# Optimization experiments

Measured on AMD Instinct MI355X. Metric: run time of the kernel, lower is better.

Reference implementation:

```python
import jax, jax.numpy as jnp
import numpy as np

B, C, H, W = 2, 192, 96, 96
HEADS, DG, KH, KW = 12, 12, 3, 3
K = KH * KW
PAD, DIL = KH // 2, 1
MLP_HIDDEN = 2 * C  # mlp_ratio = 2


def setup_inputs() -> dict:
    key = jax.random.key(0)
    ks = jax.random.split(key, 14)
    s = 0.02
    return {
        "q": jax.random.normal(ks[0], (B, C, H, W), jnp.float32),
        "k": jax.random.normal(ks[1], (B, C, H, W), jnp.float32),
        "v": jax.random.normal(ks[2], (B, C, H, W), jnp.float32),
        "offset": jax.random.normal(ks[3], (B, DG * 2 * K, H, W), jnp.float32),
        "Wq": jax.random.normal(ks[4], (C, C), jnp.float32) * s,
        "bq": jax.random.normal(ks[5], (C,), jnp.float32) * s,
        "Wk": jax.random.normal(ks[6], (C, C), jnp.float32) * s,
        "bk": jax.random.normal(ks[7], (C,), jnp.float32) * s,
        "Wv": jax.random.normal(ks[8], (C, C), jnp.float32) * s,
        "bv": jax.random.normal(ks[9], (C,), jnp.float32) * s,
        "W1": jax.random.normal(ks[10], (C, MLP_HIDDEN), jnp.float32) * s,
        "b1": jax.random.normal(ks[11], (MLP_HIDDEN,), jnp.float32) * s,
        "W2": jax.random.normal(ks[12], (MLP_HIDDEN, C), jnp.float32) * s,
        "b2": jax.random.normal(ks[13], (C,), jnp.float32) * s,
    }


def _bilinear_sample(img, py, px):
    """img: [B,G,Cg,H,W]; py,px: [B,G,K,H,W] fractional sample coords.
    Returns [B,G,Cg,K,H,W]; zero outside image (DCN-style per-corner masking)."""
    b, g, cg, h, w = img.shape
    y0 = jnp.floor(py)
    x0 = jnp.floor(px)
    wy1 = py - y0
    wx1 = px - x0
    wy0 = 1.0 - wy1
    wx0 = 1.0 - wx1
    imgf = img.reshape(b, g, cg, h * w)

    def corner(yi, xi, wgt):
        valid = ((yi >= 0) & (yi <= h - 1) & (xi >= 0) & (xi <= w - 1)).astype(img.dtype)
        yc = jnp.clip(yi, 0, h - 1).astype(jnp.int32)
        xc = jnp.clip(xi, 0, w - 1).astype(jnp.int32)
        idx = (yc * w + xc).reshape(b, g, 1, -1)  # [B,G,1,K*H*W]
        gth = jnp.take_along_axis(imgf, idx, axis=3)  # [B,G,Cg,K*H*W]
        return gth * (valid * wgt).reshape(b, g, 1, -1)

    out = (corner(y0, x0, wy0 * wx0)
           + corner(y0, x0 + 1, wy0 * wx1)
           + corner(y0 + 1, x0, wy1 * wx0)
           + corner(y0 + 1, x0 + 1, wy1 * wx1))
    return out.reshape(b, g, cg, py.shape[2], h, w)


def _forward(q, k, v, offset, Wq, bq, Wk, bk, Wv, bv, W1, b1, W2, b2):
    def lin(x, Wm, bb):  # per-pixel Linear over channel dim
        return jnp.einsum('bchw,cd->bdhw', x, Wm) + bb[None, :, None, None]

    qp = lin(q, Wq, bq)
    kp = lin(k, Wk, bk)
    vp = lin(v, Wv, bv)

    # DCN-v1 offset layout: [B, G, K, 2(y,x), H, W]
    off = offset.reshape(B, DG, K, 2, H, W)
    ii, jj = jnp.meshgrid(jnp.arange(KH), jnp.arange(KW), indexing='ij')
    ii = ii.reshape(K)
    jj = jj.reshape(K)
    base_y = (jnp.arange(H)[None, :] - PAD + (ii * DIL)[:, None]).astype(jnp.float32)  # [K,H]
    base_x = (jnp.arange(W)[None, :] - PAD + (jj * DIL)[:, None]).astype(jnp.float32)  # [K,W]
    py = base_y[None, None, :, :, None] + off[:, :, :, 0]  # [B,G,K,H,W]
    px = base_x[None, None, :, None, :] + off[:, :, :, 1]

    cg = C // DG
    k_s = _bilinear_sample(kp.reshape(B, DG, cg, H, W), py, px)  # [B,G,cg,K,H,W]
    v_s = _bilinear_sample(vp.reshape(B, DG, cg, H, W), py, px)

    hd = C // HEADS
    k_s = k_s.reshape(B, HEADS, hd, K, H, W)
    v_s = v_s.reshape(B, HEADS, hd, K, H, W)
    qh = qp.reshape(B, HEADS, hd, H, W)

    scale = hd ** -0.5
    scores = jnp.einsum('bndhw,bndkhw->bnkhw', qh, k_s) * scale
    attn = jax.nn.softmax(scores, axis=2)  # over K sampled points (clip_size=1)
    out = jnp.einsum('bnkhw,bndkhw->bndhw', attn, v_s).reshape(B, C, H, W)

    # residual MLP (GELU exact, as torch nn.GELU default)
    xf = out.transpose(0, 2, 3, 1)  # [B,H,W,C]
    h1 = jax.nn.gelu(xf @ W1 + b1, approximate=False)
    mlp = (h1 @ W2 + b2).transpose(0, 3, 1, 2)
    return out + mlp


def reference(q, k, v, offset, Wq, bq, Wk, bk, Wv, bv, W1, b1, W2, b2):
    return _forward(q, k, v, offset, Wq, bq, Wk, bk, Wv, bv, W1, b1, W2, b2)
```

## Files before the change

### kernel.cpp

```cpp
#include <hip/hip_runtime.h>
#include <hip/hip_bf16.h>
#include <math.h>

#define B_    2
#define C_    192
#define H_    96
#define W_    96
#define HW_   (H_ * W_)
#define NPIX_ (B_ * HW_)
#define G_    12
#define CG_   16
#define KPTS_ 9
#define MLPH_ 384

typedef __attribute__((ext_vector_type(8))) short s16x8;
typedef __attribute__((ext_vector_type(4))) float f32x4;

__device__ __forceinline__ ushort f2b(float f) {
    __hip_bfloat16 h = __float2bfloat16(f);
    return *reinterpret_cast<ushort*>(&h);
}
__device__ __forceinline__ float b2f(ushort u) {
    return __uint_as_float(((uint)u) << 16);
}
__device__ __forceinline__ float b2f_lo(uint u) { return __uint_as_float(u << 16); }
__device__ __forceinline__ float b2f_hi(uint u) { return __uint_as_float(u & 0xffff0000u); }

#define GLOAD16(gp, lp)                                                          \
    __builtin_amdgcn_global_load_lds(                                            \
        (const __attribute__((address_space(1))) void*)(gp),                     \
        (__attribute__((address_space(3))) void*)(lp), 16, 0, 0)

__global__ __launch_bounds__(256) void pack_kernel(
    const float* __restrict__ q, const float* __restrict__ k,
    const float* __restrict__ v, ushort* __restrict__ Xcl)
{
    __shared__ ushort sm[64][196];
    const int t   = threadIdx.x;
    const int hw0 = blockIdx.x * 64;
    const int b   = blockIdx.y;
    const int z   = blockIdx.z;
    const float* X = (z == 0) ? q : (z == 1) ? k : v;

    const int hwl = t & 63;
    #pragma unroll 4
    for (int j = 0; j < 48; ++j) {
        const int c = (t >> 6) + j * 4;
        sm[hwl][c] = f2b(X[(b * C_ + c) * HW_ + hw0 + hwl]);
    }
    __syncthreads();
    #pragma unroll
    for (int jj = 0; jj < 12; ++jj) {
        const int idx = t + 256 * jj;
        const int row = idx / 48, cq = idx - row * 48;
        const int pix = b * HW_ + hw0 + row;
        *(uint2*)&Xcl[((z * NPIX_) + pix) * C_ + cq * 4] = *(uint2*)&sm[row][cq * 4];
    }
}

__global__ __launch_bounds__(256) void wpack_kernel(
    const float* __restrict__ Wq, const float* __restrict__ Wk,
    const float* __restrict__ Wv, const float* __restrict__ W1,
    const float* __restrict__ W2, ushort* __restrict__ Wt)
{
    const int i = blockIdx.x * 256 + threadIdx.x;
    if (i < 110592) {
        const int s = i / 36864, j = i - s * 36864;
        const float* src = (s == 0) ? Wq : (s == 1) ? Wk : Wv;
        const int d = j / 192, c = j - d * 192;
        Wt[i] = f2b(src[c * 192 + d]);
    } else if (i < 184320) {
        const int j = i - 110592, d = j / 192, c = j - d * 192;
        Wt[i] = f2b(W1[c * 384 + d]);
    } else if (i < 258048) {
        const int j = i - 184320, d = j / 384, c = j - d * 384;
        Wt[i] = f2b(W2[c * 192 + d]);
    }
}

template<int KK>
__device__ __forceinline__ void stage_tiles64(const ushort* Az, const ushort* Bz,
                                              ushort* dst, int t, int m0, int n0, int kt)
{
    #pragma unroll
    for (int j = 0; j < 4; ++j) {
        const int q = t + 256 * j;
        const int r = q >> 3, p = q & 7;
        const int s = p ^ (r & 7);
        GLOAD16(Az + (size_t)(m0 + r) * KK + kt * 64 + s * 8, dst + q * 8);
    }
    #pragma unroll
    for (int j = 0; j < 2; ++j) {
        const int q = t + 256 * j;
        const int r = q >> 3, p = q & 7;
        const int s = p ^ (r & 7);
        GLOAD16(Bz + (size_t)(n0 + r) * KK + kt * 64 + s * 8, dst + 8192 + q * 8);
    }
}

template<int KK, int EPI>
__global__ __launch_bounds__(256) void gemm_kernel(
    const ushort* __restrict__ A,  const ushort* __restrict__ BT,
    const float* __restrict__ bias0, const float* __restrict__ bias1,
    const float* __restrict__ bias2,
    ushort* __restrict__ Ob,
    const ushort* __restrict__ res, float* __restrict__ Onchw,
    int zAstr, int zBstr, int zOstr)
{
    __shared__ char lds_raw[49152];
    ushort* smem = (ushort*)lds_raw;

    const int t  = threadIdx.x;
    const int l  = t & 63;
    const int wid = t >> 6;
    const int wm = wid >> 1, wn = wid & 1;
    const int m0 = blockIdx.x * 128;
    const int n0 = blockIdx.y * 64;
    const int z  = blockIdx.z;
    const int Ntot = gridDim.y * 64;
    constexpr int NKT = KK / 64;

    const ushort* Az = A  + (size_t)z * zAstr;
    const ushort* Bz = BT + (size_t)z * zBstr;
    const float* bias = (z == 0) ? bias0 : (z == 1) ? bias1 : bias2;

    int aoff[4][2], boff[2][2];
    #pragma unroll
    for (int f = 0; f < 4; ++f) {
        const int r = wm * 64 + f * 16 + (l & 15);
        #pragma unroll
        for (int ks = 0; ks < 2; ++ks) {
            const int c = ks * 4 + (l >> 4);
            aoff[f][ks] = r * 64 + (c ^ (r & 7)) * 8;
        }
    }
    #pragma unroll
    for (int g = 0; g < 2; ++g) {
        const int r = wn * 32 + g * 16 + (l & 15);
        #pragma unroll
        for (int ks = 0; ks < 2; ++ks) {
            const int c = ks * 4 + (l >> 4);
            boff[g][ks] = 8192 + r * 64 + (c ^ (r & 7)) * 8;
        }
    }

    f32x4 acc[4][2] = {};

    stage_tiles64<KK>(Az, Bz, smem, t, m0, n0, 0);
    __syncthreads();

    for (int kt = 0; kt < NKT; ++kt) {
        if (kt + 1 < NKT)
            stage_tiles64<KK>(Az, Bz, smem + ((kt + 1) & 1) * 12288, t, m0, n0, kt + 1);

        const ushort* buf = smem + (kt & 1) * 12288;
        s16x8 af[4][2], bf[2][2];
        #pragma unroll
        for (int f = 0; f < 4; ++f)
            #pragma unroll
            for (int ks = 0; ks < 2; ++ks) af[f][ks] = *(const s16x8*)(buf + aoff[f][ks]);
        #pragma unroll
        for (int g = 0; g < 2; ++g)
            #pragma unroll
            for (int ks = 0; ks < 2; ++ks) bf[g][ks] = *(const s16x8*)(buf + boff[g][ks]);
        #pragma unroll
        for (int ks = 0; ks < 2; ++ks)
            #pragma unroll
            for (int f = 0; f < 4; ++f)
                #pragma unroll
                for (int g = 0; g < 2; ++g)
                    acc[f][g] = __builtin_amdgcn_mfma_f32_16x16x32_bf16(af[f][ks], bf[g][ks], acc[f][g], 0, 0, 0);
        __syncthreads();
    }

    const int rowg = l >> 4, ncol = l & 15;
    float bv[2];
    #pragma unroll
    for (int g = 0; g < 2; ++g) bv[g] = bias[n0 + wn * 32 + g * 16 + ncol];

    if (EPI == 0) {
        ushort* O = Ob + (size_t)z * zOstr;
        #pragma unroll
        for (int f = 0; f < 4; ++f)
            #pragma unroll
            for (int g = 0; g < 2; ++g)
                #pragma unroll
                for (int r = 0; r < 4; ++r) {
                    const int m = m0 + wm * 64 + f * 16 + rowg * 4 + r;
                    const int n = n0 + wn * 32 + g * 16 + ncol;
                    O[(size_t)m * Ntot + n] = f2b(acc[f][g][r] + bv[g]);
                }
    } else if (EPI == 1) {
        #pragma unroll
        for (int f = 0; f < 4; ++f)
            #pragma unroll
            for (int g = 0; g < 2; ++g)
                #pragma unroll
                for (int r = 0; r < 4; ++r) {
                    const int m = m0 + wm * 64 + f * 16 + rowg * 4 + r;
                    const int n = n0 + wn * 32 + g * 16 + ncol;
                    const float x = acc[f][g][r] + bv[g];
                    Ob[(size_t)m * Ntot + n] = f2b(0.5f * x * (1.f + erff(x * 0.70710678118f)));
                }
    } else {
        float* tsp = (float*)lds_raw;
        #pragma unroll
        for (int f = 0; f < 4; ++f)
            #pragma unroll
            for (int g = 0; g < 2; ++g)
                #pragma unroll
                for (int r = 0; r < 4; ++r) {
                    const int ml = wm * 64 + f * 16 + rowg * 4 + r;
                    const int nl = wn * 32 + g * 16 + ncol;
                    const float rv = b2f(res[(size_t)(m0 + ml) * C_ + n0 + nl]);
                    tsp[nl * 132 + ml] = acc[f][g][r] + bv[g] + rv;
                }
        __syncthreads();
        const int b   = m0 / HW_;
        const int hw0 = m0 - b * HW_;
        #pragma unroll
        for (int jj = 0; jj < 8; ++jj) {
            const int i4 = t + 256 * jj;
            const int nn = i4 >> 5, mc = i4 & 31;
            float4 val = *(float4*)&tsp[nn * 132 + mc * 4];
            *(float4*)&Onchw[(size_t)b * C_ * HW_ + (size_t)(n0 + nn) * HW_ + hw0 + mc * 4] = val;
        }
    }
}

__global__ __launch_bounds__(256, 2) void deform_attn_kernel(
    const ushort* __restrict__ qp, const ushort* __restrict__ kp,
    const ushort* __restrict__ vp, const float* __restrict__ offset,
    ushort* __restrict__ aob)
{
    const int t   = threadIdx.x;
    const int bid = blockIdx.x;
    const int xb  = (bid & 7) * 432 + (bid >> 3);
    const int pair = xb * 64 + (t >> 2);
    const int lane4 = t & 3;
    const int g   = pair % G_;
    const int pix = pair / G_;
    const int b   = pix / HW_;
    const int hw  = pix - b * HW_;
    const int h   = hw / W_;
    const int w   = hw - h * W_;
    const int gc0 = g * CG_ + lane4 * 4;

    float q0, q1, q2, q3;
    {
        uint2 qu = *(const uint2*)(qp + pix * C_ + gc0);
        q0 = b2f_lo(qu.x); q1 = b2f_hi(qu.x);
        q2 = b2f_lo(qu.y); q3 = b2f_hi(qu.y);
    }

    float offy[3] = {0.f, 0.f, 0.f}, offx[3] = {0.f, 0.f, 0.f};
    {
        const int obase = (b * (G_ * 2 * KPTS_) + g * (2 * KPTS_)) * HW_ + hw;
        #pragma unroll
        for (int s = 0; s < 3; ++s) {
            const int kk = lane4 + s * 4;
            if (kk < KPTS_) {
                offy[s] = offset[obase + (kk * 2) * HW_];
                offx[s] = offset[obase + (kk * 2 + 1) * HW_];
            }
        }
    }

    int   addr[KPTS_][4];
    float wgt[KPTS_][4];
    #pragma unroll
    for (int kk = 0; kk < KPTS_; ++kk) {
        const float oy = __shfl(offy[kk >> 2], kk & 3, 4);
        const float ox = __shfl(offx[kk >> 2], kk & 3, 4);
        const float py = (float)(h - 1 + kk / 3) + oy;
        const float px = (float)(w - 1 + kk % 3) + ox;
        const float fy = floorf(py), fx = floorf(px);
        const int   y0 = (int)fy,   x0 = (int)fx;
        const float wy1 = py - fy, wx1 = px - fx;
        const float wy0 = 1.f - wy1, wx0 = 1.f - wx1;

        const float wy0m = ((unsigned)y0       < (unsigned)H_) ? wy0 : 0.f;
        const float wy1m = ((unsigned)(y0 + 1) < (unsigned)H_) ? wy1 : 0.f;
        const float wx0m = ((unsigned)x0       < (unsigned)W_) ? wx0 : 0.f;
        const float wx1m = ((unsigned)(x0 + 1) < (unsigned)W_) ? wx1 : 0.f;
        const int yc0 = min(max(y0, 0), H_ - 1);
        const int yc1 = min(max(y0 + 1, 0), H_ - 1);
        const int xc0 = min(max(x0, 0), W_ - 1);
        const int xc1 = min(max(x0 + 1, 0), W_ - 1);

        addr[kk][0] = (yc0 * W_ + xc0) * C_ + gc0;  wgt[kk][0] = wy0m * wx0m;
        addr[kk][1] = (yc0 * W_ + xc1) * C_ + gc0;  wgt[kk][1] = wy0m * wx1m;
        addr[kk][2] = (yc1 * W_ + xc0) * C_ + gc0;  wgt[kk][2] = wy1m * wx0m;
        addr[kk][3] = (yc1 * W_ + xc1) * C_ + gc0;  wgt[kk][3] = wy1m * wx1m;
    }

    const ushort* kp_b = kp + (size_t)b * HW_ * C_;
    const ushort* vp_b = vp + (size_t)b * HW_ * C_;

    float score[KPTS_];
    #pragma unroll
    for (int kk = 0; kk < KPTS_; ++kk) {
        float s = 0.f;
        #pragma unroll
        for (int c = 0; c < 4; ++c) {
            const uint2 ku = *(const uint2*)(kp_b + addr[kk][c]);
            float d = q0 * b2f_lo(ku.x);
            d = fmaf(q1, b2f_hi(ku.x), d);
            d = fmaf(q2, b2f_lo(ku.y), d);
            d = fmaf(q3, b2f_hi(ku.y), d);
            s = fmaf(wgt[kk][c], d, s);
        }
        score[kk] = s;
    }
    #pragma unroll
    for (int kk = 0; kk < KPTS_; ++kk) {
        float sc = score[kk];
        sc += __shfl_xor(sc, 1, 4);
        sc += __shfl_xor(sc, 2, 4);
        score[kk] = sc * 0.25f;
    }

    float m = score[0];
    #pragma unroll
    for (int kk = 1; kk < KPTS_; ++kk) m = fmaxf(m, score[kk]);
    float ssum = 0.f;
    #pragma unroll
    for (int kk = 0; kk < KPTS_; ++kk) { score[kk] = __expf(score[kk] - m); ssum += score[kk]; }
    const float inv = 1.f / ssum;

    f32x4 o = {0.f, 0.f, 0.f, 0.f};
    #pragma unroll
    for (int kk = 0; kk < KPTS_; ++kk) {
        const float p = score[kk] * inv;
        #pragma unroll
        for (int c = 0; c < 4; ++c) {
            const float pw = p * wgt[kk][c];
            const uint2 vu = *(const uint2*)(vp_b + addr[kk][c]);
            o[0] = fmaf(pw, b2f_lo(vu.x), o[0]);
            o[1] = fmaf(pw, b2f_hi(vu.x), o[1]);
            o[2] = fmaf(pw, b2f_lo(vu.y), o[2]);
            o[3] = fmaf(pw, b2f_hi(vu.y), o[3]);
        }
    }

    uint2 ob;
    ob.x = (uint)f2b(o[0]) | ((uint)f2b(o[1]) << 16);
    ob.y = (uint)f2b(o[2]) | ((uint)f2b(o[3]) << 16);
    *(uint2*)(aob + pix * C_ + gc0) = ob;
}

extern "C" void kernel_launch(void* const* d_in, const int* in_sizes, int n_in,
                              void* d_out, int out_size, void* d_ws, size_t ws_size,
                              hipStream_t stream)
{
    const float* q      = (const float*)d_in[0];
    const float* k      = (const float*)d_in[1];
    const float* v      = (const float*)d_in[2];
    const float* offset = (const float*)d_in[3];
    const float* Wq     = (const float*)d_in[4];
    const float* bq     = (const float*)d_in[5];
    const float* Wk     = (const float*)d_in[6];
    const float* bk     = (const float*)d_in[7];
    const float* Wv     = (const float*)d_in[8];
    const float* bv     = (const float*)d_in[9];
    const float* W1     = (const float*)d_in[10];
    const float* b1     = (const float*)d_in[11];
    const float* W2     = (const float*)d_in[12];
    const float* b2     = (const float*)d_in[13];

    ushort* Xcl = (ushort*)d_ws;
    ushort* aob = Xcl;
    ushort* qkv = Xcl + 3 * NPIX_ * C_;
    ushort* Hb  = qkv + 3 * NPIX_ * C_;
    ushort* Wt  = Hb + (size_t)NPIX_ * MLPH_;
    ushort* W1T = Wt + 110592;
    ushort* W2T = Wt + 184320;

    pack_kernel<<<dim3(HW_ / 64, B_, 3), 256, 0, stream>>>(q, k, v, Xcl);
    wpack_kernel<<<1008, 256, 0, stream>>>(Wq, Wk, Wv, W1, W2, Wt);

    gemm_kernel<192, 0><<<dim3(NPIX_ / 128, 3, 3), 256, 0, stream>>>(
        Xcl, Wt, bq, bk, bv, qkv, nullptr, nullptr,
        NPIX_ * C_, C_ * C_, NPIX_ * C_);

    deform_attn_kernel<<<NPIX_ * G_ / 64, 256, 0, stream>>>(
        qkv, qkv + NPIX_ * C_, qkv + 2 * NPIX_ * C_, offset, aob);

    gemm_kernel<192, 1><<<dim3(NPIX_ / 128, 6, 1), 256, 0, stream>>>(
        aob, W1T, b1, b1, b1, Hb, nullptr, nullptr, 0, 0, 0);

    gemm_kernel<384, 2><<<dim3(NPIX_ / 128, 3, 1), 256, 0, stream>>>(
        Hb, W2T, b2, b2, b2, nullptr, aob, (float*)d_out, 0, 0, 0);
}
```

Before: 200.7 us.

## Drop LDS staging in GEMM, prefetch V gathers, use bf16 dot2 for scores

The GEMM kernel no longer stages tiles through shared memory with double buffering. Each wave now loads MFMA fragments straight from global memory, and launch bounds allow two blocks per CU. The deformable-attention kernel issues all 36 V gathers up front, before the score pass, to overlap their latency, and computes q·k with the bf16 fdot2 intrinsic when it is available. The trade is more redundant global and L2 traffic in the GEMMs and higher register pressure from holding all V values.

```diff
diff --git a/kernel.cpp b/kernel.cpp
--- a/kernel.cpp
+++ b/kernel.cpp
@@ -26,10 +26,16 @@
 __device__ __forceinline__ float b2f_lo(uint u) { return __uint_as_float(u << 16); }
 __device__ __forceinline__ float b2f_hi(uint u) { return __uint_as_float(u & 0xffff0000u); }
 
-#define GLOAD16(gp, lp)                                                          \
-    __builtin_amdgcn_global_load_lds(                                            \
-        (const __attribute__((address_space(1))) void*)(gp),                     \
-        (__attribute__((address_space(3))) void*)(lp), 16, 0, 0)
+#if __has_builtin(__builtin_amdgcn_fdot2_f32_bf16)
+typedef __attribute__((ext_vector_type(2))) __bf16 bf16x2;
+#define HAVE_DOT2BF 1
+__device__ __forceinline__ float dot2bf(uint a, uint b, float c) {
+    return __builtin_amdgcn_fdot2_f32_bf16(__builtin_bit_cast(bf16x2, a),
+                                           __builtin_bit_cast(bf16x2, b), c, false);
+}
+#else
+#define HAVE_DOT2BF 0
+#endif
 
 __global__ __launch_bounds__(256) void pack_kernel(
     const float* __restrict__ q, const float* __restrict__ k,
@@ -78,28 +84,8 @@
     }
 }
 
-template<int KK>
-__device__ __forceinline__ void stage_tiles64(const ushort* Az, const ushort* Bz,
-                                              ushort* dst, int t, int m0, int n0, int kt)
-{
-    #pragma unroll
-    for (int j = 0; j < 4; ++j) {
-        const int q = t + 256 * j;
-        const int r = q >> 3, p = q & 7;
-        const int s = p ^ (r & 7);
-        GLOAD16(Az + (size_t)(m0 + r) * KK + kt * 64 + s * 8, dst + q * 8);
-    }
-    #pragma unroll
-    for (int j = 0; j < 2; ++j) {
-        const int q = t + 256 * j;
-        const int r = q >> 3, p = q & 7;
-        const int s = p ^ (r & 7);
-        GLOAD16(Bz + (size_t)(n0 + r) * KK + kt * 64 + s * 8, dst + 8192 + q * 8);
-    }
-}
-
 template<int KK, int EPI>
-__global__ __launch_bounds__(256) void gemm_kernel(
+__global__ __launch_bounds__(256, 2) void gemm_kernel(
     const ushort* __restrict__ A,  const ushort* __restrict__ BT,
     const float* __restrict__ bias0, const float* __restrict__ bias1,
     const float* __restrict__ bias2,
@@ -107,9 +93,6 @@
     const ushort* __restrict__ res, float* __restrict__ Onchw,
     int zAstr, int zBstr, int zOstr)
 {
-    __shared__ char lds_raw[49152];
-    ushort* smem = (ushort*)lds_raw;
-
     const int t  = threadIdx.x;
     const int l  = t & 63;
     const int wid = t >> 6;
@@ -118,59 +101,35 @@
     const int n0 = blockIdx.y * 64;
     const int z  = blockIdx.z;
     const int Ntot = gridDim.y * 64;
-    constexpr int NKT = KK / 64;
 
     const ushort* Az = A  + (size_t)z * zAstr;
     const ushort* Bz = BT + (size_t)z * zBstr;
     const float* bias = (z == 0) ? bias0 : (z == 1) ? bias1 : bias2;
 
-    int aoff[4][2], boff[2][2];
-    #pragma unroll
-    for (int f = 0; f < 4; ++f) {
-        const int r = wm * 64 + f * 16 + (l & 15);
-        #pragma unroll
-        for (int ks = 0; ks < 2; ++ks) {
-            const int c = ks * 4 + (l >> 4);
-            aoff[f][ks] = r * 64 + (c ^ (r & 7)) * 8;
-        }
-    }
-    #pragma unroll
-    for (int g = 0; g < 2; ++g) {
-        const int r = wn * 32 + g * 16 + (l & 15);
-        #pragma unroll
-        for (int ks = 0; ks < 2; ++ks) {
-            const int c = ks * 4 + (l >> 4);
-            boff[g][ks] = 8192 + r * 64 + (c ^ (r & 7)) * 8;
-        }
-    }
+    const int lr = l & 15, lc = (l >> 4) * 8;
+    const ushort* pa[4];
+    #pragma unroll
+    for (int f = 0; f < 4; ++f)
+        pa[f] = Az + (size_t)(m0 + wm * 64 + f * 16 + lr) * KK + lc;
+    const ushort* pb[2];
+    #pragma unroll
+    for (int g = 0; g < 2; ++g)
+        pb[g] = Bz + (size_t)(n0 + wn * 32 + g * 16 + lr) * KK + lc;
 
     f32x4 acc[4][2] = {};
 
-    stage_tiles64<KK>(Az, Bz, smem, t, m0, n0, 0);
-    __syncthreads();
-
-    for (int kt = 0; kt < NKT; ++kt) {
-        if (kt + 1 < NKT)
-            stage_tiles64<KK>(Az, Bz, smem + ((kt + 1) & 1) * 12288, t, m0, n0, kt + 1);
-
-        const ushort* buf = smem + (kt & 1) * 12288;
-        s16x8 af[4][2], bf[2][2];
+    #pragma unroll
+    for (int ks = 0; ks < KK / 32; ++ks) {
+        s16x8 af[4], bf[2];
+        #pragma unroll
+        for (int f = 0; f < 4; ++f) af[f] = *(const s16x8*)(pa[f] + ks * 32);
+        #pragma unroll
+        for (int g = 0; g < 2; ++g) bf[g] = *(const s16x8*)(pb[g] + ks * 32);
         #pragma unroll
         for (int f = 0; f < 4; ++f)
             #pragma unroll
-            for (int ks = 0; ks < 2; ++ks) af[f][ks] = *(const s16x8*)(buf + aoff[f][ks]);
-        #pragma unroll
-        for (int g = 0; g < 2; ++g)
-            #pragma unroll
-            for (int ks = 0; ks < 2; ++ks) bf[g][ks] = *(const s16x8*)(buf + boff[g][ks]);
-        #pragma unroll
-        for (int ks = 0; ks < 2; ++ks)
-            #pragma unroll
-            for (int f = 0; f < 4; ++f)
-                #pragma unroll
-                for (int g = 0; g < 2; ++g)
-                    acc[f][g] = __builtin_amdgcn_mfma_f32_16x16x32_bf16(af[f][ks], bf[g][ks], acc[f][g], 0, 0, 0);
-        __syncthreads();
+            for (int g = 0; g < 2; ++g)
+                acc[f][g] = __builtin_amdgcn_mfma_f32_16x16x32_bf16(af[f], bf[g], acc[f][g], 0, 0, 0);
     }
 
     const int rowg = l >> 4, ncol = l & 15;
@@ -178,7 +137,7 @@
     #pragma unroll
     for (int g = 0; g < 2; ++g) bv[g] = bias[n0 + wn * 32 + g * 16 + ncol];
 
-    if (EPI == 0) {
+    if constexpr (EPI == 0) {
         ushort* O = Ob + (size_t)z * zOstr;
         #pragma unroll
         for (int f = 0; f < 4; ++f)
@@ -190,7 +149,7 @@
                     const int n = n0 + wn * 32 + g * 16 + ncol;
                     O[(size_t)m * Ntot + n] = f2b(acc[f][g][r] + bv[g]);
                 }
-    } else if (EPI == 1) {
+    } else if constexpr (EPI == 1) {
         #pragma unroll
         for (int f = 0; f < 4; ++f)
             #pragma unroll
@@ -203,7 +162,7 @@
                     Ob[(size_t)m * Ntot + n] = f2b(0.5f * x * (1.f + erff(x * 0.70710678118f)));
                 }
     } else {
-        float* tsp = (float*)lds_raw;
+        __shared__ float tsp[64][132];
         #pragma unroll
         for (int f = 0; f < 4; ++f)
             #pragma unroll
@@ -213,7 +172,7 @@
                     const int ml = wm * 64 + f * 16 + rowg * 4 + r;
                     const int nl = wn * 32 + g * 16 + ncol;
                     const float rv = b2f(res[(size_t)(m0 + ml) * C_ + n0 + nl]);
-                    tsp[nl * 132 + ml] = acc[f][g][r] + bv[g] + rv;
+                    tsp[nl][ml] = acc[f][g][r] + bv[g] + rv;
                 }
         __syncthreads();
         const int b   = m0 / HW_;
@@ -222,7 +181,7 @@
         for (int jj = 0; jj < 8; ++jj) {
             const int i4 = t + 256 * jj;
             const int nn = i4 >> 5, mc = i4 & 31;
-            float4 val = *(float4*)&tsp[nn * 132 + mc * 4];
+            float4 val = *(float4*)&tsp[nn][mc * 4];
             *(float4*)&Onchw[(size_t)b * C_ * HW_ + (size_t)(n0 + nn) * HW_ + hw0 + mc * 4] = val;
         }
     }
@@ -246,12 +205,9 @@
     const int w   = hw - h * W_;
     const int gc0 = g * CG_ + lane4 * 4;
 
-    float q0, q1, q2, q3;
-    {
-        uint2 qu = *(const uint2*)(qp + pix * C_ + gc0);
-        q0 = b2f_lo(qu.x); q1 = b2f_hi(qu.x);
-        q2 = b2f_lo(qu.y); q3 = b2f_hi(qu.y);
-    }
+    uint2 qu = *(const uint2*)(qp + pix * C_ + gc0);
+    const float q0 = b2f_lo(qu.x), q1 = b2f_hi(qu.x);
+    const float q2 = b2f_lo(qu.y), q3 = b2f_hi(qu.y);
 
     float offy[3] = {0.f, 0.f, 0.f}, offx[3] = {0.f, 0.f, 0.f};
     {
@@ -297,6 +253,13 @@
     const ushort* kp_b = kp + (size_t)b * HW_ * C_;
     const ushort* vp_b = vp + (size_t)b * HW_ * C_;
 
+    uint2 vu[KPTS_][4];
+    #pragma unroll
+    for (int kk = 0; kk < KPTS_; ++kk)
+        #pragma unroll
+        for (int c = 0; c < 4; ++c)
+            vu[kk][c] = *(const uint2*)(vp_b + addr[kk][c]);
+
     float score[KPTS_];
     #pragma unroll
     for (int kk = 0; kk < KPTS_; ++kk) {
@@ -304,10 +267,14 @@
         #pragma unroll
         for (int c = 0; c < 4; ++c) {
             const uint2 ku = *(const uint2*)(kp_b + addr[kk][c]);
+#if HAVE_DOT2BF
+            const float d = dot2bf(ku.y, qu.y, dot2bf(ku.x, qu.x, 0.f));
+#else
             float d = q0 * b2f_lo(ku.x);
             d = fmaf(q1, b2f_hi(ku.x), d);
             d = fmaf(q2, b2f_lo(ku.y), d);
             d = fmaf(q3, b2f_hi(ku.y), d);
+#endif
             s = fmaf(wgt[kk][c], d, s);
         }
         score[kk] = s;
@@ -335,11 +302,10 @@
         #pragma unroll
         for (int c = 0; c < 4; ++c) {
             const float pw = p * wgt[kk][c];
-            const uint2 vu = *(const uint2*)(vp_b + addr[kk][c]);
-            o[0] = fmaf(pw, b2f_lo(vu.x), o[0]);
-            o[1] = fmaf(pw, b2f_hi(vu.x), o[1]);
-            o[2] = fmaf(pw, b2f_lo(vu.y), o[2]);
-            o[3] = fmaf(pw, b2f_hi(vu.y), o[3]);
+            o[0] = fmaf(pw, b2f_lo(vu[kk][c].x), o[0]);
+            o[1] = fmaf(pw, b2f_hi(vu[kk][c].x), o[1]);
+            o[2] = fmaf(pw, b2f_lo(vu[kk][c].y), o[2]);
+            o[3] = fmaf(pw, b2f_hi(vu[kk][c].y), o[3]);
         }
     }
 
```

After: 238.0 us. 18.6% more time.
